# Performance work log

Hardware: AMD Instinct MI355X
Metric: run time of the kernel (lower is better)

## Reference

```python
import jax, jax.numpy as jnp
import numpy as np

EMBED_DIM = 1024
NUM_HEADS = 16
HEAD_DIM = EMBED_DIM // NUM_HEADS


def setup_inputs() -> dict:
    key = jax.random.key(0)
    k_x, k_wqkv, k_bqkv, k_wout, k_bout = jax.random.split(key, 5)
    B, T, C = 2, 2048, EMBED_DIM
    s = 1.0 / np.sqrt(C)
    return {
        "x": jax.random.normal(k_x, (B, T, C), dtype=jnp.float32),
        "W_qkv": jax.random.uniform(k_wqkv, (C, 3 * C), jnp.float32, -s, s),
        "b_qkv": jax.random.uniform(k_bqkv, (3 * C,), jnp.float32, -s, s),
        "W_out": jax.random.uniform(k_wout, (C, C), jnp.float32, -s, s),
        "b_out": jax.random.uniform(k_bout, (C,), jnp.float32, -s, s),
    }


def reference(x, W_qkv, b_qkv, W_out, b_out):
    B, T, C = x.shape
    H, D = NUM_HEADS, HEAD_DIM
    qkv = x @ W_qkv + b_qkv                      # [B,T,3C]
    # Faithful to torch: reshape to [B,T,H,3D], move heads, chunk last dim.
    qkv = qkv.reshape(B, T, H, 3 * D).transpose(0, 2, 1, 3)  # [B,H,T,3D]
    q, k, v = qkv[..., :D], qkv[..., D:2 * D], qkv[..., 2 * D:]
    scores = jnp.einsum("bhqd,bhkd->bhqk", q, k) / np.sqrt(D).astype(jnp.float32)
    weights = jax.nn.softmax(scores, axis=-1)    # [B,H,T,T]
    attn = jnp.einsum("bhqk,bhkd->bhqd", weights, v)  # [B,H,T,D]
    attn = attn.transpose(0, 2, 1, 3).reshape(B, T, C)
    return attn @ W_out + b_out
```

## Files before the change

kernel.cpp:

```cpp
#include <hip/hip_runtime.h>


typedef float  f32x4  __attribute__((ext_vector_type(4)));
typedef __bf16 bf16x8 __attribute__((ext_vector_type(8)));
typedef __bf16 bf16x4 __attribute__((ext_vector_type(4)));

#define QSCALE 0.18033688011112042f

static __device__ __forceinline__ f32x4 mfma32(bf16x8 a, bf16x8 b, f32x4 c) {
    return __builtin_amdgcn_mfma_f32_16x16x32_bf16(a, b, c, 0, 0, 0);
}

static __device__ __forceinline__ bf16x8 ld8(const unsigned short* p) {
    return __builtin_bit_cast(bf16x8, *(const uint4*)p);
}
static __device__ __forceinline__ unsigned short bfbits(float f) {
    __bf16 h = (__bf16)f;
    return __builtin_bit_cast(unsigned short, h);
}

static __device__ __forceinline__ void glds16(const unsigned short* g,
                                              unsigned short* lds_base) {
    __builtin_amdgcn_global_load_lds(
        (const __attribute__((address_space(1))) unsigned int*)g,
        (__attribute__((address_space(3))) unsigned int*)lds_base, 16, 0, 0);
}

__global__ __launch_bounds__(256) void cast_x_kernel(
    const float* __restrict__ x, unsigned short* __restrict__ xb) {
    int i = blockIdx.x * 256 + threadIdx.x;
    float4 v = ((const float4*)x)[i];
    ushort4 o;
    o.x = bfbits(v.x); o.y = bfbits(v.y); o.z = bfbits(v.z); o.w = bfbits(v.w);
    ((ushort4*)xb)[i] = o;
}

__global__ __launch_bounds__(256) void transpose_cast_kernel(
    const float* __restrict__ W, unsigned short* __restrict__ Wt, int K, int N) {
    __shared__ float tile[32][33];
    int tx = threadIdx.x & 31, ty = threadIdx.x >> 5;
    int n0 = blockIdx.x * 32, k0 = blockIdx.y * 32;
#pragma unroll
    for (int i = 0; i < 4; i++) {
        int r = ty + i * 8;
        tile[r][tx] = W[(size_t)(k0 + r) * N + n0 + tx];
    }
    __syncthreads();
#pragma unroll
    for (int i = 0; i < 4; i++) {
        int r = ty + i * 8;
        Wt[(size_t)(n0 + r) * K + k0 + tx] = bfbits(tile[tx][r]);
    }
}

__global__ __launch_bounds__(256) void qkv_gemm_kernel(
    const unsigned short* __restrict__ A, const unsigned short* __restrict__ Bt,
    const float* __restrict__ bias, unsigned short* __restrict__ Qb,
    unsigned short* __restrict__ Kb, unsigned short* __restrict__ Vtb) {
    __shared__ unsigned short As[2][128 * 32];
    __shared__ unsigned short Bs[2][128 * 32];
    const int wg = blockIdx.x;
    const int xcd = wg & 7, local = wg >> 3;
    const int n_t = (xcd >> 2) * 12 + local % 12;
    const int m_t = (xcd & 3) * 8 + local / 12;
    const int m0 = m_t * 128, n0 = n_t * 128;
    const int tid = threadIdx.x;
    const int lane = tid & 63, w = tid >> 6;
    const int ln = lane & 15, quad = lane >> 4;
    const int wm = (w >> 1) * 64, wn = (w & 1) * 64;
    const int sr = lane >> 2, sc = (lane & 3) * 8;
    f32x4 acc[4][4] = {};
#pragma unroll
    for (int i = 0; i < 2; i++) {
        int r0 = w * 32 + i * 16;
        glds16(&A[(size_t)(m0 + r0 + sr) * 1024 + sc], &As[0][r0 * 32]);
        glds16(&Bt[(size_t)(n0 + r0 + sr) * 1024 + sc], &Bs[0][r0 * 32]);
    }
    __syncthreads();
    for (int kt = 0; kt < 32; kt++) {
        const int cur = kt & 1;
        if (kt + 1 < 32) {
            const int nxt = cur ^ 1;
            const int kc = (kt + 1) * 32;
#pragma unroll
            for (int i = 0; i < 2; i++) {
                int r0 = w * 32 + i * 16;
                glds16(&A[(size_t)(m0 + r0 + sr) * 1024 + kc + sc], &As[nxt][r0 * 32]);
                glds16(&Bt[(size_t)(n0 + r0 + sr) * 1024 + kc + sc], &Bs[nxt][r0 * 32]);
            }
        }
        bf16x8 af[4], bf[4];
#pragma unroll
        for (int mi = 0; mi < 4; mi++)
            af[mi] = ld8(&As[cur][(wm + mi * 16 + ln) * 32 + quad * 8]);
#pragma unroll
        for (int ni = 0; ni < 4; ni++)
            bf[ni] = ld8(&Bs[cur][(wn + ni * 16 + ln) * 32 + quad * 8]);
#pragma unroll
        for (int mi = 0; mi < 4; mi++)
#pragma unroll
            for (int ni = 0; ni < 4; ni++)
                acc[mi][ni] = mfma32(af[mi], bf[ni], acc[mi][ni]);
        __syncthreads();
    }
#pragma unroll
    for (int mi = 0; mi < 4; mi++)
#pragma unroll
        for (int ni = 0; ni < 4; ni++) {
            int gn = n0 + wn + ni * 16 + ln;
            float bi = bias[gn];
            int h = gn / 192, rr = gn - h * 192;
#pragma unroll
            for (int r = 0; r < 4; r++) {
                int gm = m0 + wm + mi * 16 + quad * 4 + r;
                float v = acc[mi][ni][r] + bi;
                int b = gm >> 11, t = gm & 2047;
                size_t base = ((size_t)(b * 16 + h) * 2048 + t) * 64;
                if (rr < 64)        Qb[base + rr] = bfbits(v * QSCALE);
                else if (rr < 128)  Kb[base + rr - 64] = bfbits(v);
                else {
                    int tp = (t & ~31) | ((t & 0x0C) << 1) | ((t & 0x10) >> 2)
                           | (t & 3);
                    Vtb[((size_t)(b * 16 + h) * 64 + (rr - 128)) * 2048 + tp]
                        = bfbits(v);
                }
            }
        }
}

__global__ __launch_bounds__(512)
__attribute__((amdgpu_waves_per_eu(4, 4)))
void attn_kernel(
    const unsigned short* __restrict__ Q, const unsigned short* __restrict__ K,
    const unsigned short* __restrict__ Vt, unsigned short* __restrict__ Ob) {
    __shared__ unsigned short smem[2][2][2][4096];
    const int wg  = blockIdx.x;
    const int xcd = wg & 7, local = wg >> 3;
    const int bh  = xcd * 4 + (local >> 4);
    const int qt  = local & 15;
    const int tid = threadIdx.x;
    const int lane = tid & 63, w = tid >> 6;
    const int w4 = w & 3, ks = w >> 2;
    const int ln = lane & 15, quad = lane >> 4;
    const int lr = lane >> 3, lg = lane & 7;
    const int e = ln & 7;

    unsigned short (*Ks)[4096] = smem[ks][0];
    unsigned short (*Vs)[4096] = smem[ks][1];

    const unsigned short* Qg = Q + ((size_t)bh * 2048 + qt * 128) * 64;
    const unsigned short* Kg = K + ((size_t)bh * 2048 + ks * 1024) * 64;
    const unsigned short* Vg = Vt + (size_t)bh * 64 * 2048 + ks * 1024;

    bf16x8 qf[2][2];
#pragma unroll
    for (int h = 0; h < 2; h++) {
        const unsigned short* qp = Qg + (size_t)(w4 * 32 + h * 16 + ln) * 64;
        qf[h][0] = ld8(qp + quad * 8);
        qf[h][1] = ld8(qp + 32 + quad * 8);
    }

    const unsigned short* kb0 = &Ks[0][ln * 64 + (quad ^ e) * 8];
    const unsigned short* kb1 = &Ks[0][ln * 64 + ((4 + quad) ^ e) * 8];
    const unsigned short* vp0 = &Vs[0][ln * 64 + (quad ^ e) * 8];
    const unsigned short* vp1 = &Vs[0][ln * 64 + ((4 + quad) ^ e) * 8];

    const int kof0 = (w4 * 16 + lr) * 64 + (lg ^ lr) * 8;
    const int kof1 = (w4 * 16 + 8 + lr) * 64 + (lg ^ lr) * 8;
    const int vof0 = (w4 * 16 + lr) * 2048 + (lg ^ lr) * 8;
    const int vof1 = (w4 * 16 + 8 + lr) * 2048 + (lg ^ lr) * 8;
    unsigned short* kd0[2] = {&Ks[0][(w4 * 16) * 64], &Ks[1][(w4 * 16) * 64]};
    unsigned short* kd1[2] = {&Ks[0][(w4 * 16 + 8) * 64], &Ks[1][(w4 * 16 + 8) * 64]};
    unsigned short* vd0[2] = {&Vs[0][(w4 * 16) * 64], &Vs[1][(w4 * 16) * 64]};
    unsigned short* vd1[2] = {&Vs[0][(w4 * 16 + 8) * 64], &Vs[1][(w4 * 16 + 8) * 64]};

    glds16(Kg + kof0, kd0[0]);
    glds16(Kg + kof1, kd1[0]);
    glds16(Vg + vof0, vd0[0]);
    glds16(Vg + vof1, vd1[0]);
    __syncthreads();

    const unsigned short* KgR = Kg + 4096;
    const unsigned short* VgR = Vg + 64;

    bf16x8 ones8;
#pragma unroll
    for (int j = 0; j < 8; j++) ones8[j] = __bf16(1.0f);
    f32x4 o[2][4] = {};
    f32x4 lacc[2] = {};

#define ATTN_TILE(CUR, PREF)                                                  \
    do {                                                                      \
        if (PREF) {                                                           \
            glds16(KgR + kof0, kd0[CUR ^ 1]);                                 \
            glds16(KgR + kof1, kd1[CUR ^ 1]);                                 \
            glds16(VgR + vof0, vd0[CUR ^ 1]);                                 \
            glds16(VgR + vof1, vd1[CUR ^ 1]);                                 \
            KgR += 4096; VgR += 64;                                           \
        }                                                                     \
        f32x4 s[2][4] = {};                                                   \
        _Pragma("unroll")                                                     \
        for (int ms = 0; ms < 4; ms++) {                                      \
            bf16x8 a0 = ld8(kb0 + (CUR) * 4096 + ms * 1024);                  \
            bf16x8 a1 = ld8(kb1 + (CUR) * 4096 + ms * 1024);                  \
            _Pragma("unroll")                                                 \
            for (int h = 0; h < 2; h++) {                                     \
                s[h][ms] = mfma32(a0, qf[h][0], s[h][ms]);                    \
                s[h][ms] = mfma32(a1, qf[h][1], s[h][ms]);                    \
            }                                                                 \
        }                                                                     \
            \
            \
        bf16x8 pb8[2][2];                                                     \
        _Pragma("unroll")                                                     \
        for (int h = 0; h < 2; h++)                                           \
            _Pragma("unroll")                                                 \
            for (int p = 0; p < 2; p++) {                                     \
                f32x4 e0, e1;                                                 \
                e0[0] = exp2f(s[h][2 * p][0]); e0[1] = exp2f(s[h][2 * p][1]); \
                e0[2] = exp2f(s[h][2 * p][2]); e0[3] = exp2f(s[h][2 * p][3]); \
                e1[0] = exp2f(s[h][2 * p + 1][0]);                            \
                e1[1] = exp2f(s[h][2 * p + 1][1]);                            \
                e1[2] = exp2f(s[h][2 * p + 1][2]);                            \
                e1[3] = exp2f(s[h][2 * p + 1][3]);                            \
                pb8[h][p][0] = __bf16(e0[0]); pb8[h][p][1] = __bf16(e0[1]);   \
                pb8[h][p][2] = __bf16(e0[2]); pb8[h][p][3] = __bf16(e0[3]);   \
                pb8[h][p][4] = __bf16(e1[0]); pb8[h][p][5] = __bf16(e1[1]);   \
                pb8[h][p][6] = __bf16(e1[2]); pb8[h][p][7] = __bf16(e1[3]);   \
            }                                                                 \
        _Pragma("unroll")                                                     \
        for (int h = 0; h < 2; h++)                                           \
            _Pragma("unroll")                                                 \
            for (int p = 0; p < 2; p++)                                       \
                lacc[h] = mfma32(ones8, pb8[h][p], lacc[h]);                  \
        _Pragma("unroll")                                                     \
        for (int df = 0; df < 4; df++) {                                      \
            bf16x8 a80 = ld8(vp0 + (CUR) * 4096 + df * 1024);                 \
            o[0][df] = mfma32(a80, pb8[0][0], o[0][df]);                      \
            o[1][df] = mfma32(a80, pb8[1][0], o[1][df]);                      \
            bf16x8 a81 = ld8(vp1 + (CUR) * 4096 + df * 1024);                 \
            o[0][df] = mfma32(a81, pb8[0][1], o[0][df]);                      \
            o[1][df] = mfma32(a81, pb8[1][1], o[1][df]);                      \
        }                                                                     \
        __syncthreads();                                                      \
    } while (0)

    for (int it = 0; it < 8; it++) {
        ATTN_TILE(0, true);
        ATTN_TILE(1, (it < 7));
    }
#undef ATTN_TILE

    float* xf = (float*)&smem[0][0][0][0];
    const int slot = w4 * 64 + lane;
    if (ks) {
#pragma unroll
        for (int h = 0; h < 2; h++)
#pragma unroll
            for (int df = 0; df < 4; df++) {
                int j = h * 4 + df;
                *(f32x4*)(xf + (size_t)(slot * 8 + (j ^ (slot & 7))) * 4) = o[h][df];
            }
        xf[8192 + slot * 2 + 0] = lacc[0][0];
        xf[8192 + slot * 2 + 1] = lacc[1][0];
    }
    __syncthreads();
    if (!ks) {
        float inv0 = 1.0f / (lacc[0][0] + xf[8192 + slot * 2 + 0]);
        float inv1 = 1.0f / (lacc[1][0] + xf[8192 + slot * 2 + 1]);
        const int b = bh >> 4, hh = bh & 15;
#pragma unroll
        for (int h = 0; h < 2; h++) {
            float inv = h ? inv1 : inv0;
            int qrow = qt * 128 + w4 * 32 + h * 16 + ln;
            size_t row = ((size_t)b * 2048 + qrow) * 1024 + hh * 64;
#pragma unroll
            for (int df = 0; df < 4; df++) {
                int j = h * 4 + df;
                f32x4 oo = *(const f32x4*)(xf + (size_t)(slot * 8 + (j ^ (slot & 7))) * 4);
                ushort4 pk;
                pk.x = bfbits((o[h][df][0] + oo[0]) * inv);
                pk.y = bfbits((o[h][df][1] + oo[1]) * inv);
                pk.z = bfbits((o[h][df][2] + oo[2]) * inv);
                pk.w = bfbits((o[h][df][3] + oo[3]) * inv);
                *(ushort4*)&Ob[row + df * 16 + quad * 4] = pk;
            }
        }
    }
}

__global__ __launch_bounds__(256) void out_gemm_kernel(
    const unsigned short* __restrict__ A, const unsigned short* __restrict__ Bt,
    const float* __restrict__ bias, float* __restrict__ out) {
    __shared__ unsigned short As[2][128 * 32];
    __shared__ unsigned short Bs[2][128 * 32];
    const int wg = blockIdx.x;
    const int xcd = wg & 7, local = wg >> 3;
    const int n_t = (xcd >> 2) * 4 + (local & 3);
    const int m_t = (xcd & 3) * 8 + (local >> 2);
    const int m0 = m_t * 128, n0 = n_t * 128;
    const int tid = threadIdx.x;
    const int lane = tid & 63, w = tid >> 6;
    const int ln = lane & 15, quad = lane >> 4;
    const int wm = (w >> 1) * 64, wn = (w & 1) * 64;
    const int sr = lane >> 2, sc = (lane & 3) * 8;
    f32x4 acc[4][4] = {};
#pragma unroll
    for (int i = 0; i < 2; i++) {
        int r0 = w * 32 + i * 16;
        glds16(&A[(size_t)(m0 + r0 + sr) * 1024 + sc], &As[0][r0 * 32]);
        glds16(&Bt[(size_t)(n0 + r0 + sr) * 1024 + sc], &Bs[0][r0 * 32]);
    }
    __syncthreads();
    for (int kt = 0; kt < 32; kt++) {
        const int cur = kt & 1;
        if (kt + 1 < 32) {
            const int nxt = cur ^ 1;
            const int kc = (kt + 1) * 32;
#pragma unroll
            for (int i = 0; i < 2; i++) {
                int r0 = w * 32 + i * 16;
                glds16(&A[(size_t)(m0 + r0 + sr) * 1024 + kc + sc], &As[nxt][r0 * 32]);
                glds16(&Bt[(size_t)(n0 + r0 + sr) * 1024 + kc + sc], &Bs[nxt][r0 * 32]);
            }
        }
        bf16x8 af[4], bf[4];
#pragma unroll
        for (int mi = 0; mi < 4; mi++)
            af[mi] = ld8(&As[cur][(wm + mi * 16 + ln) * 32 + quad * 8]);
#pragma unroll
        for (int ni = 0; ni < 4; ni++)
            bf[ni] = ld8(&Bs[cur][(wn + ni * 16 + ln) * 32 + quad * 8]);
#pragma unroll
        for (int mi = 0; mi < 4; mi++)
#pragma unroll
            for (int ni = 0; ni < 4; ni++)
                acc[mi][ni] = mfma32(af[mi], bf[ni], acc[mi][ni]);
        __syncthreads();
    }
#pragma unroll
    for (int mi = 0; mi < 4; mi++)
#pragma unroll
        for (int ni = 0; ni < 4; ni++) {
            int gn = n0 + wn + ni * 16 + ln;
            float bi = bias[gn];
#pragma unroll
            for (int r = 0; r < 4; r++) {
                int gm = m0 + wm + mi * 16 + quad * 4 + r;
                out[(size_t)gm * 1024 + gn] = acc[mi][ni][r] + bi;
            }
        }
}

extern "C" void kernel_launch(void* const* d_in, const int* in_sizes, int n_in,
                              void* d_out, int out_size, void* d_ws, size_t ws_size,
                              hipStream_t stream) {
    const float* x     = (const float*)d_in[0];
    const float* W_qkv = (const float*)d_in[1];
    const float* b_qkv = (const float*)d_in[2];
    const float* W_out = (const float*)d_in[3];
    const float* b_out = (const float*)d_in[4];
    float* out = (float*)d_out;

    char* ws = (char*)d_ws;
    unsigned short* xb    = (unsigned short*)(ws);
    unsigned short* wqkvT = (unsigned short*)(ws + (size_t)( 8 << 20));
    unsigned short* woutT = (unsigned short*)(ws + (size_t)(14 << 20));
    unsigned short* Qb    = (unsigned short*)(ws + (size_t)(16 << 20));
    unsigned short* Kb    = (unsigned short*)(ws + (size_t)(24 << 20));
    unsigned short* Vtb   = (unsigned short*)(ws + (size_t)(32 << 20));
    unsigned short* attnb = (unsigned short*)(ws + (size_t)(40 << 20));

    cast_x_kernel<<<4096, 256, 0, stream>>>(x, xb);
    transpose_cast_kernel<<<dim3(96, 32), 256, 0, stream>>>(W_qkv, wqkvT, 1024, 3072);
    transpose_cast_kernel<<<dim3(32, 32), 256, 0, stream>>>(W_out, woutT, 1024, 1024);
    qkv_gemm_kernel<<<768, 256, 0, stream>>>(xb, wqkvT, b_qkv, Qb, Kb, Vtb);
    attn_kernel<<<512, 512, 0, stream>>>(Qb, Kb, Vtb, attnb);
    out_gemm_kernel<<<256, 256, 0, stream>>>(attnb, woutT, b_out, out);
}
```

Measured before the change: 207.0 us.

## Merge prep kernels, vectorize V-transpose stores, halve out-GEMM M tile

Result: faster. 191.7 us (-7.4%).

```diff
diff --git a/kernel.cpp b/kernel.cpp
--- a/kernel.cpp
+++ b/kernel.cpp
@@ -3,7 +3,6 @@
 
 typedef float  f32x4  __attribute__((ext_vector_type(4)));
 typedef __bf16 bf16x8 __attribute__((ext_vector_type(8)));
-typedef __bf16 bf16x4 __attribute__((ext_vector_type(4)));
 
 #define QSCALE 0.18033688011112042f
 
@@ -26,20 +25,30 @@
         (__attribute__((address_space(3))) unsigned int*)lds_base, 16, 0, 0);
 }
 
-__global__ __launch_bounds__(256) void cast_x_kernel(
-    const float* __restrict__ x, unsigned short* __restrict__ xb) {
-    int i = blockIdx.x * 256 + threadIdx.x;
-    float4 v = ((const float4*)x)[i];
-    ushort4 o;
-    o.x = bfbits(v.x); o.y = bfbits(v.y); o.z = bfbits(v.z); o.w = bfbits(v.w);
-    ((ushort4*)xb)[i] = o;
-}
-
-__global__ __launch_bounds__(256) void transpose_cast_kernel(
-    const float* __restrict__ W, unsigned short* __restrict__ Wt, int K, int N) {
+__global__ __launch_bounds__(256) void prep_kernel(
+    const float* __restrict__ x, unsigned short* __restrict__ xb,
+    const float* __restrict__ Wqkv, unsigned short* __restrict__ wqkvT,
+    const float* __restrict__ Wout, unsigned short* __restrict__ woutT) {
     __shared__ float tile[32][33];
+    const int bid = blockIdx.x;
+    if (bid < 4096) {
+        int i = bid * 256 + threadIdx.x;
+        float4 v = ((const float4*)x)[i];
+        ushort4 o;
+        o.x = bfbits(v.x); o.y = bfbits(v.y);
+        o.z = bfbits(v.z); o.w = bfbits(v.w);
+        ((ushort4*)xb)[i] = o;
+        return;
+    }
+    const float* W; unsigned short* Wt; int N, n0, k0;
+    if (bid < 7168) {
+        int l = bid - 4096; W = Wqkv; Wt = wqkvT; N = 3072;
+        n0 = (l % 96) * 32; k0 = (l / 96) * 32;
+    } else {
+        int l = bid - 7168; W = Wout; Wt = woutT; N = 1024;
+        n0 = (l & 31) * 32; k0 = (l >> 5) * 32;
+    }
     int tx = threadIdx.x & 31, ty = threadIdx.x >> 5;
-    int n0 = blockIdx.x * 32, k0 = blockIdx.y * 32;
 #pragma unroll
     for (int i = 0; i < 4; i++) {
         int r = ty + i * 8;
@@ -49,7 +58,7 @@
 #pragma unroll
     for (int i = 0; i < 4; i++) {
         int r = ty + i * 8;
-        Wt[(size_t)(n0 + r) * K + k0 + tx] = bfbits(tile[tx][r]);
+        Wt[(size_t)(n0 + r) * 1024 + k0 + tx] = bfbits(tile[tx][r]);
     }
 }
 
@@ -110,20 +119,28 @@
             int gn = n0 + wn + ni * 16 + ln;
             float bi = bias[gn];
             int h = gn / 192, rr = gn - h * 192;
-#pragma unroll
-            for (int r = 0; r < 4; r++) {
-                int gm = m0 + wm + mi * 16 + quad * 4 + r;
-                float v = acc[mi][ni][r] + bi;
-                int b = gm >> 11, t = gm & 2047;
-                size_t base = ((size_t)(b * 16 + h) * 2048 + t) * 64;
-                if (rr < 64)        Qb[base + rr] = bfbits(v * QSCALE);
-                else if (rr < 128)  Kb[base + rr - 64] = bfbits(v);
-                else {
-                    int tp = (t & ~31) | ((t & 0x0C) << 1) | ((t & 0x10) >> 2)
-                           | (t & 3);
-                    Vtb[((size_t)(b * 16 + h) * 64 + (rr - 128)) * 2048 + tp]
-                        = bfbits(v);
-                }
+            int gm0 = m0 + wm + mi * 16 + quad * 4;
+            int b = gm0 >> 11, t0 = gm0 & 2047;
+            float vv[4];
+#pragma unroll
+            for (int r = 0; r < 4; r++) vv[r] = acc[mi][ni][r] + bi;
+            if (rr < 64) {
+                size_t base = ((size_t)(b * 16 + h) * 2048 + t0) * 64 + rr;
+#pragma unroll
+                for (int r = 0; r < 4; r++)
+                    Qb[base + (size_t)r * 64] = bfbits(vv[r] * QSCALE);
+            } else if (rr < 128) {
+                size_t base = ((size_t)(b * 16 + h) * 2048 + t0) * 64 + rr - 64;
+#pragma unroll
+                for (int r = 0; r < 4; r++)
+                    Kb[base + (size_t)r * 64] = bfbits(vv[r]);
+            } else {
+                int tp0 = (t0 & ~31) | (quad << 3) | ((mi & 1) << 2);
+                ushort4 pk;
+                pk.x = bfbits(vv[0]); pk.y = bfbits(vv[1]);
+                pk.z = bfbits(vv[2]); pk.w = bfbits(vv[3]);
+                *(ushort4*)&Vtb[((size_t)(b * 16 + h) * 64 + (rr - 128)) * 2048
+                                + tp0] = pk;
             }
         }
 }
@@ -209,8 +226,6 @@
                 s[h][ms] = mfma32(a1, qf[h][1], s[h][ms]);                    \
             }                                                                 \
         }                                                                     \
-            \
-            \
         bf16x8 pb8[2][2];                                                     \
         _Pragma("unroll")                                                     \
         for (int h = 0; h < 2; h++)                                           \
@@ -292,24 +307,27 @@
 __global__ __launch_bounds__(256) void out_gemm_kernel(
     const unsigned short* __restrict__ A, const unsigned short* __restrict__ Bt,
     const float* __restrict__ bias, float* __restrict__ out) {
-    __shared__ unsigned short As[2][128 * 32];
+    __shared__ unsigned short As[2][64 * 32];
     __shared__ unsigned short Bs[2][128 * 32];
     const int wg = blockIdx.x;
     const int xcd = wg & 7, local = wg >> 3;
-    const int n_t = (xcd >> 2) * 4 + (local & 3);
-    const int m_t = (xcd & 3) * 8 + (local >> 2);
-    const int m0 = m_t * 128, n0 = n_t * 128;
+    const int m_t = xcd * 8 + (local & 7);
+    const int n_t = local >> 3;
+    const int m0 = m_t * 64, n0 = n_t * 128;
     const int tid = threadIdx.x;
     const int lane = tid & 63, w = tid >> 6;
     const int ln = lane & 15, quad = lane >> 4;
-    const int wm = (w >> 1) * 64, wn = (w & 1) * 64;
+    const int wm = (w >> 1) * 32, wn = (w & 1) * 64;
     const int sr = lane >> 2, sc = (lane & 3) * 8;
-    f32x4 acc[4][4] = {};
-#pragma unroll
-    for (int i = 0; i < 2; i++) {
-        int r0 = w * 32 + i * 16;
-        glds16(&A[(size_t)(m0 + r0 + sr) * 1024 + sc], &As[0][r0 * 32]);
-        glds16(&Bt[(size_t)(n0 + r0 + sr) * 1024 + sc], &Bs[0][r0 * 32]);
+    f32x4 acc[2][4] = {};
+    {
+        int ra = w * 16;
+        glds16(&A[(size_t)(m0 + ra + sr) * 1024 + sc], &As[0][ra * 32]);
+#pragma unroll
+        for (int i = 0; i < 2; i++) {
+            int rb = w * 32 + i * 16;
+            glds16(&Bt[(size_t)(n0 + rb + sr) * 1024 + sc], &Bs[0][rb * 32]);
+        }
     }
     __syncthreads();
     for (int kt = 0; kt < 32; kt++) {
@@ -317,29 +335,30 @@
         if (kt + 1 < 32) {
             const int nxt = cur ^ 1;
             const int kc = (kt + 1) * 32;
+            int ra = w * 16;
+            glds16(&A[(size_t)(m0 + ra + sr) * 1024 + kc + sc], &As[nxt][ra * 32]);
 #pragma unroll
             for (int i = 0; i < 2; i++) {
-                int r0 = w * 32 + i * 16;
-                glds16(&A[(size_t)(m0 + r0 + sr) * 1024 + kc + sc], &As[nxt][r0 * 32]);
-                glds16(&Bt[(size_t)(n0 + r0 + sr) * 1024 + kc + sc], &Bs[nxt][r0 * 32]);
-            }
-        }
-        bf16x8 af[4], bf[4];
-#pragma unroll
-        for (int mi = 0; mi < 4; mi++)
+                int rb = w * 32 + i * 16;
+                glds16(&Bt[(size_t)(n0 + rb + sr) * 1024 + kc + sc], &Bs[nxt][rb * 32]);
+            }
+        }
+        bf16x8 af[2], bf[4];
+#pragma unroll
+        for (int mi = 0; mi < 2; mi++)
             af[mi] = ld8(&As[cur][(wm + mi * 16 + ln) * 32 + quad * 8]);
 #pragma unroll
         for (int ni = 0; ni < 4; ni++)
             bf[ni] = ld8(&Bs[cur][(wn + ni * 16 + ln) * 32 + quad * 8]);
 #pragma unroll
-        for (int mi = 0; mi < 4; mi++)
+        for (int mi = 0; mi < 2; mi++)
 #pragma unroll
             for (int ni = 0; ni < 4; ni++)
                 acc[mi][ni] = mfma32(af[mi], bf[ni], acc[mi][ni]);
         __syncthreads();
     }
 #pragma unroll
-    for (int mi = 0; mi < 4; mi++)
+    for (int mi = 0; mi < 2; mi++)
 #pragma unroll
         for (int ni = 0; ni < 4; ni++) {
             int gn = n0 + wn + ni * 16 + ln;
@@ -371,10 +390,8 @@
     unsigned short* Vtb   = (unsigned short*)(ws + (size_t)(32 << 20));
     unsigned short* attnb = (unsigned short*)(ws + (size_t)(40 << 20));
 
-    cast_x_kernel<<<4096, 256, 0, stream>>>(x, xb);
-    transpose_cast_kernel<<<dim3(96, 32), 256, 0, stream>>>(W_qkv, wqkvT, 1024, 3072);
-    transpose_cast_kernel<<<dim3(32, 32), 256, 0, stream>>>(W_out, woutT, 1024, 1024);
+    prep_kernel<<<8192, 256, 0, stream>>>(x, xb, W_qkv, wqkvT, W_out, woutT);
     qkv_gemm_kernel<<<768, 256, 0, stream>>>(xb, wqkvT, b_qkv, Qb, Kb, Vtb);
     attn_kernel<<<512, 512, 0, stream>>>(Qb, Kb, Vtb, attnb);
-    out_gemm_kernel<<<256, 256, 0, stream>>>(attnb, woutT, b_out, out);
-}
+    out_gemm_kernel<<<512, 256, 0, stream>>>(attnb, woutT, b_out, out);
+}
```
